# Kernel optimization log

Hardware: AMD Instinct MI355X
Metric: run time of the kernel (lower is better)

## Reference

```python
import jax, jax.numpy as jnp
import numpy as np

B, C, H, W = 4, 256, 64, 64
C8 = C // 8


def setup_inputs() -> dict:
    key = jax.random.key(0)
    k1, k2, k3, k4 = jax.random.split(key, 4)
    x = jax.random.normal(k1, (B, C, H, W), dtype=jnp.float32)
    # conv1d(ks=1, bias=False) projections -> plain [out, in] matrices
    Wq = jax.random.normal(k2, (C8, C), dtype=jnp.float32) * (1.0 / np.sqrt(C))
    Wk = jax.random.normal(k3, (C8, C), dtype=jnp.float32) * (1.0 / np.sqrt(C))
    Wv = jax.random.normal(k4, (C, C), dtype=jnp.float32) * (1.0 / np.sqrt(C))
    gamma = jnp.zeros((1,), dtype=jnp.float32)
    return {"x": x, "Wq": Wq, "Wk": Wk, "Wv": Wv, "gamma": gamma}


def reference(x, Wq, Wk, Wv, gamma):
    b, c, h, w = x.shape
    xf = x.reshape(b, c, h * w)                      # [B, C, N]
    f = jnp.einsum('oc,bcn->bon', Wq, xf)            # [B, C/8, N] query
    g = jnp.einsum('oc,bcn->bon', Wk, xf)            # [B, C/8, N] key
    hv = jnp.einsum('oc,bcn->bon', Wv, xf)           # [B, C,   N] value
    # scores[b,i,j] = sum_c f[b,c,i] * g[b,c,j]; softmax over dim=1 (i)
    scores = jnp.einsum('bci,bcj->bij', f, g)        # [B, N, N]
    beta = jax.nn.softmax(scores, axis=1)
    # o[b,c,j] = sum_i hv[b,c,i] * beta[b,i,j]
    o = jnp.einsum('bci,bij->bcj', hv, beta)         # [B, C, N]
    out = gamma[0] * o + xf
    return out.reshape(b, c, h, w)
```

## Files before the change

### kernel.cpp

```cpp
#include <hip/hip_runtime.h>

#define B_  4
#define C_  256
#define C8_ 32
#define N_  4096
#define HVS_ (N_ + 64)

#define TJ 128
#define KI 128
#define SPLITS 4

typedef __attribute__((ext_vector_type(8)))  short bf16x8;
typedef __attribute__((ext_vector_type(16))) float f32x16;

union FragAB { bf16x8 v; unsigned short u[8]; };

__device__ __forceinline__ unsigned short f2bf(float x) {
    unsigned u = __float_as_uint(x);
    unsigned r = u + 0x7FFFu + ((u >> 16) & 1u);
    return (unsigned short)(r >> 16);
}
__device__ __forceinline__ unsigned pack2bf(float a, float b) {
    return (unsigned)f2bf(a) | ((unsigned)f2bf(b) << 16);
}
__device__ __forceinline__ unsigned cvtpk(float lo, float hi) {
    unsigned r;
    asm("v_cvt_pk_bf16_f32 %0, %1, %2" : "=v"(r) : "v"(lo), "v"(hi));
    return r;
}

__global__ __launch_bounds__(256) void prep_w_kernel(
    const float* __restrict__ Wq, const float* __restrict__ Wk,
    const float* __restrict__ Wv, unsigned short* __restrict__ Wbf)
{
    int idx = (blockIdx.x * 256 + threadIdx.x) * 4;
    int row = idx >> 8;
    int col = idx & 255;
    const float* src; int r;
    if (row < 32)      { src = Wq; r = row;      }
    else if (row < 64) { src = Wk; r = row - 32; }
    else               { src = Wv; r = row - 64; }
    float4 v = *(const float4*)&src[r * 256 + col];
    uint2 o; o.x = pack2bf(v.x, v.y); o.y = pack2bf(v.z, v.w);
    *(uint2*)&Wbf[idx] = o;
}

__global__ __launch_bounds__(256) void prep_x_kernel(
    const float* __restrict__ x, unsigned short* __restrict__ xT)
{
    __shared__ unsigned short T[64][66];
    int t  = threadIdx.x;
    int b  = blockIdx.z;
    int c0 = blockIdx.y * 64;
    int n0 = blockIdx.x * 64;
    const float* xb = x + (size_t)b * C_ * N_;
    int n_l = t & 63, c_l = t >> 6;
#pragma unroll
    for (int q = 0; q < 16; ++q) {
        int c = c_l * 16 + q;
        T[n_l][c] = f2bf(xb[(size_t)(c0 + c) * N_ + n0 + n_l]);
    }
    __syncthreads();
    unsigned short* xTb = xT + (size_t)b * N_ * C_;
    int c_l2 = t & 63, nb = t >> 6;
#pragma unroll
    for (int q = 0; q < 16; ++q) {
        int n = nb * 16 + q;
        xTb[(size_t)(n0 + n) * C_ + c0 + c_l2] = T[n][c_l2];
    }
}

__global__ __launch_bounds__(256) void proj_mfma_kernel(
    const unsigned short* __restrict__ Wbf, const unsigned short* __restrict__ xT,
    unsigned short* __restrict__ fT, unsigned short* __restrict__ g,
    unsigned short* __restrict__ hv)
{
    int t = threadIdx.x, w = t >> 6, lane = t & 63;
    int half = lane >> 5, l31 = lane & 31;
    int b  = blockIdx.y;
    int n0 = blockIdx.x * 32;

    const unsigned short* xb = xT + ((size_t)b * N_ + n0 + l31) * C_;
    int nm = (w < 2) ? 3 : 2;
    int mt0 = w, mt1 = w + 4, mt2 = w + 8;

    f32x16 acc[3];
#pragma unroll
    for (int a = 0; a < 3; ++a) acc[a] = (f32x16)0.f;

#pragma unroll
    for (int ks = 0; ks < 16; ++ks) {
        int kofs = ks * 16 + half * 8;
        bf16x8 bfr = *(const bf16x8*)&xb[kofs];
        bf16x8 a0 = *(const bf16x8*)&Wbf[(size_t)(mt0 * 32 + l31) * 256 + kofs];
        acc[0] = __builtin_amdgcn_mfma_f32_32x32x16_bf16(a0, bfr, acc[0], 0, 0, 0);
        bf16x8 a1 = *(const bf16x8*)&Wbf[(size_t)(mt1 * 32 + l31) * 256 + kofs];
        acc[1] = __builtin_amdgcn_mfma_f32_32x32x16_bf16(a1, bfr, acc[1], 0, 0, 0);
        if (nm == 3) {
            bf16x8 a2 = *(const bf16x8*)&Wbf[(size_t)(mt2 * 32 + l31) * 256 + kofs];
            acc[2] = __builtin_amdgcn_mfma_f32_32x32x16_bf16(a2, bfr, acc[2], 0, 0, 0);
        }
    }

    unsigned short* fTb = fT + (size_t)b * N_ * C8_;
    unsigned short* gb  = g  + (size_t)b * C8_ * N_;
    unsigned short* hb  = hv + (size_t)b * C_  * HVS_;
#pragma unroll
    for (int im = 0; im < 3; ++im) {
        if (im >= nm) break;
        int mt = (im == 0) ? mt0 : (im == 1) ? mt1 : mt2;
        if (mt == 0) {
#pragma unroll
            for (int rp = 0; rp < 8; ++rp) {
                int r = 2 * rp;
                int R = (r & 3) + 8 * (r >> 2) + 4 * half;
                unsigned u = pack2bf(acc[0][r], acc[0][r + 1]);
                *(unsigned*)&fTb[(size_t)(n0 + l31) * C8_ + R] = u;
            }
        } else {
#pragma unroll
            for (int r = 0; r < 16; ++r) {
                int R = mt * 32 + (r & 3) + 8 * (r >> 2) + 4 * half;
                unsigned short v = f2bf(acc[im][r]);
                if (R < 64) gb[(size_t)(R - 32) * N_ + n0 + l31] = v;
                else        hb[(size_t)(R - 64) * HVS_ + n0 + l31] = v;
            }
        }
    }
}

__global__ __launch_bounds__(256, 2) void flash_kernel(
    const unsigned short* __restrict__ fT, const unsigned short* __restrict__ g,
    const unsigned short* __restrict__ hv, unsigned short* __restrict__ o_part,
    float* __restrict__ l_part)
{
    __shared__ unsigned short pT[TJ * KI];

    int t = threadIdx.x, w = t >> 6, lane = t & 63;
    int half = lane >> 5, l31 = lane & 31;

    int d  = blockIdx.x;
    int jb = (d >> 3) & 31;
    int p  = (d & 7) | (((d >> 8) & 1) << 3);
    int b  = p & 3;
    int s  = p >> 2;
    int j0 = jb * TJ;

    const unsigned short* fb = fT + (size_t)b * N_ * C8_;
    const unsigned short* gb = g  + (size_t)b * C8_ * N_;
    const unsigned short* hb = hv + (size_t)b * C_  * HVS_;

    FragAB gf[2];
#pragma unroll
    for (int ks = 0; ks < 2; ++ks)
#pragma unroll
        for (int r = 0; r < 8; ++r) {
            int ch = ks * 16 + half * 8 + r;
            gf[ks].u[r] = gb[(size_t)ch * N_ + j0 + w * 32 + l31];
        }

    f32x16 acc[8];
#pragma unroll
    for (int a = 0; a < 8; ++a) acc[a] = (f32x16)0.f;
    float lacc = 0.f;

    const int swz = (l31 & 15) << 4;
    const unsigned pbase = (unsigned)(w * 32 + l31) * (KI * 2);
    char* pTc = (char*)pT;

    const unsigned short* h0 = hb + (size_t)(w * 64 + l31) * HVS_ + half * 8;
    const unsigned short* h1 = h0 + (size_t)32 * HVS_;

    int i_begin = s * (N_ / SPLITS);

    for (int ii = 0; ii < N_ / SPLITS; ii += KI) {
        int i0 = i_begin + ii;

#pragma unroll
        for (int it = 0; it < 4; ++it) {
            const unsigned short* fr = fb + (size_t)(i0 + it * 32 + l31) * C8_ + half * 8;
            bf16x8 a0 = *(const bf16x8*)fr;
            bf16x8 a1 = *(const bf16x8*)(fr + 16);
            f32x16 sacc = (f32x16)0.f;
            sacc = __builtin_amdgcn_mfma_f32_32x32x16_bf16(a0, gf[0].v, sacc, 0, 0, 0);
            sacc = __builtin_amdgcn_mfma_f32_32x32x16_bf16(a1, gf[1].v, sacc, 0, 0, 0);
            float pv[16];
#pragma unroll
            for (int r = 0; r < 16; ++r) {
                pv[r] = __expf(sacc[r]);
                lacc += pv[r];
            }
#pragma unroll
            for (int a = 0; a < 4; ++a) {
                uint2 u;
                u.x = cvtpk(pv[4 * a + 0], pv[4 * a + 1]);
                u.y = cvtpk(pv[4 * a + 2], pv[4 * a + 3]);
                int ib = ((it * 64 + a * 16) ^ swz) + half * 8;
                *(uint2*)(pTc + pbase + ib) = u;
            }
        }
        __syncthreads();

        const unsigned short* hp0 = h0 + i0;
        const unsigned short* hp1 = h1 + i0;
#pragma unroll
        for (int ks = 0; ks < 8; ++ks) {
            bf16x8 ah0 = *(const bf16x8*)(hp0 + ks * 16);
            bf16x8 ah1 = *(const bf16x8*)(hp1 + ks * 16);
            int ib = (ks * 32 + half * 16) ^ swz;
            bf16x8 bp[4];
#pragma unroll
            for (int jt = 0; jt < 4; ++jt)
                bp[jt] = *(const bf16x8*)(pTc + (jt * 32 + l31) * (KI * 2) + ib);
#pragma unroll
            for (int jt = 0; jt < 4; ++jt) {
                acc[jt]     = __builtin_amdgcn_mfma_f32_32x32x16_bf16(ah0, bp[jt], acc[jt], 0, 0, 0);
                acc[4 + jt] = __builtin_amdgcn_mfma_f32_32x32x16_bf16(ah1, bp[jt], acc[4 + jt], 0, 0, 0);
            }
        }
        __syncthreads();
    }

    unsigned short* ob = o_part + (size_t)(b * SPLITS + s) * C_ * N_;
#pragma unroll
    for (int ct = 0; ct < 2; ++ct)
#pragma unroll
        for (int jt = 0; jt < 4; ++jt) {
            f32x16 a = acc[ct * 4 + jt];
#pragma unroll
            for (int rp = 0; rp < 8; ++rp) {
                int r = 2 * rp;
                unsigned u = cvtpk(a[r], a[r + 1]);
                int c = w * 64 + ct * 32 + (r & 3) + 8 * (r >> 2) + 4 * half;
                size_t base = (size_t)c * N_ + j0 + jt * 32 + l31;
                ob[base]      = (unsigned short)(u & 0xffffu);
                ob[base + N_] = (unsigned short)(u >> 16);
            }
        }
    float lsum = lacc + __shfl_down(lacc, 32);
    if (lane < 32)
        l_part[(size_t)(b * SPLITS + s) * N_ + j0 + w * 32 + lane] = lsum;
}

__global__ __launch_bounds__(256) void combine_kernel(
    const unsigned short* __restrict__ o_part, const float* __restrict__ l_part,
    const float* __restrict__ x, const float* __restrict__ gamma,
    float* __restrict__ out)
{
    int j = (blockIdx.x * 256 + threadIdx.x) * 4;
    int b = blockIdx.z;
    float4 l4 = {0.f, 0.f, 0.f, 0.f};
#pragma unroll
    for (int s = 0; s < SPLITS; ++s) {
        float4 lv = *(const float4*)&l_part[(size_t)(b * SPLITS + s) * N_ + j];
        l4.x += lv.x; l4.y += lv.y; l4.z += lv.z; l4.w += lv.w;
    }
    float4 inv = {1.f / l4.x, 1.f / l4.y, 1.f / l4.z, 1.f / l4.w};
    float gm = gamma[0];
#pragma unroll
    for (int cc = 0; cc < 4; ++cc) {
        int c = blockIdx.y * 4 + cc;
        float4 o = {0.f, 0.f, 0.f, 0.f};
#pragma unroll
        for (int s = 0; s < SPLITS; ++s) {
            uint2 u = *(const uint2*)&o_part[((size_t)(b * SPLITS + s) * C_ + c) * N_ + j];
            o.x += __uint_as_float(u.x << 16);
            o.y += __uint_as_float(u.x & 0xffff0000u);
            o.z += __uint_as_float(u.y << 16);
            o.w += __uint_as_float(u.y & 0xffff0000u);
        }
        size_t idx = ((size_t)b * C_ + c) * N_ + j;
        float4 xv = *(const float4*)&x[idx];
        float4 st = {gm * o.x * inv.x + xv.x, gm * o.y * inv.y + xv.y,
                     gm * o.z * inv.z + xv.z, gm * o.w * inv.w + xv.w};
        *(float4*)&out[idx] = st;
    }
}

extern "C" void kernel_launch(void* const* d_in, const int* in_sizes, int n_in,
                              void* d_out, int out_size, void* d_ws, size_t ws_size,
                              hipStream_t stream) {
    const float* x     = (const float*)d_in[0];
    const float* Wq    = (const float*)d_in[1];
    const float* Wk    = (const float*)d_in[2];
    const float* Wv    = (const float*)d_in[3];
    const float* gamma = (const float*)d_in[4];
    float* out = (float*)d_out;

    char* ws = (char*)d_ws;
    unsigned short* o_part = (unsigned short*)ws;
    float* l_part = (float*)(o_part + (size_t)SPLITS * B_ * C_ * N_);
    unsigned short* fT  = (unsigned short*)(l_part + (size_t)SPLITS * B_ * N_);
    unsigned short* g   = fT  + (size_t)B_ * C8_ * N_;
    unsigned short* hv  = g   + (size_t)B_ * C8_ * N_;
    unsigned short* Wbf = hv  + (size_t)B_ * C_  * HVS_;
    unsigned short* xT  = Wbf + (size_t)(C_ + 2 * C8_) * C_;

    prep_w_kernel<<<dim3(80), 256, 0, stream>>>(Wq, Wk, Wv, Wbf);
    prep_x_kernel<<<dim3(N_ / 64, C_ / 64, B_), 256, 0, stream>>>(x, xT);

    proj_mfma_kernel<<<dim3(N_ / 32, B_), 256, 0, stream>>>(Wbf, xT, fT, g, hv);

    flash_kernel<<<dim3(512), 256, 0, stream>>>(fT, g, hv, o_part, l_part);

    combine_kernel<<<dim3(N_ / 1024, C_ / 4, B_), 256, 0, stream>>>(o_part, l_part, x, gamma, out);
}
```

Measured before the change: 160.0 us.

## Retile flash kernel to 64-column blocks with double-buffered P and packed output

Halves the attention j-tile to 64 columns, which doubles the block count to 1024, and splits waves so that each computes half of the score tile. The P tile is double-buffered in shared memory, so each iteration needs one barrier instead of two, and value fragments are preloaded into registers before the barrier. An s_setprio hint is set around the MFMA loop. Partial outputs are stored as packed bf16 pairs of channels so the stores and the combine loads are wider. The prep and projection kernels also get vectorized transpose stores and hoisted x-fragment loads. Smaller tiles reload the value data more often and raise register pressure.

Measured after the change: 175.7 us. 1.1x slower.

```diff
diff --git a/kernel.cpp b/kernel.cpp
--- a/kernel.cpp
+++ b/kernel.cpp
@@ -6,7 +6,7 @@
 #define N_  4096
 #define HVS_ (N_ + 64)
 
-#define TJ 128
+#define TJ 64
 #define KI 128
 #define SPLITS 4
 
@@ -62,11 +62,15 @@
     }
     __syncthreads();
     unsigned short* xTb = xT + (size_t)b * N_ * C_;
-    int c_l2 = t & 63, nb = t >> 6;
-#pragma unroll
-    for (int q = 0; q < 16; ++q) {
-        int n = nb * 16 + q;
-        xTb[(size_t)(n0 + n) * C_ + c0 + c_l2] = T[n][c_l2];
+    int c4 = (t & 15) * 4;
+    int nbase = t >> 4;
+#pragma unroll
+    for (int q = 0; q < 4; ++q) {
+        int n = nbase + 16 * q;
+        uint2 u;
+        u.x = (unsigned)T[n][c4]     | ((unsigned)T[n][c4 + 1] << 16);
+        u.y = (unsigned)T[n][c4 + 2] | ((unsigned)T[n][c4 + 3] << 16);
+        *(uint2*)&xTb[(size_t)(n0 + n) * C_ + c0 + c4] = u;
     }
 }
 
@@ -84,6 +88,11 @@
     int nm = (w < 2) ? 3 : 2;
     int mt0 = w, mt1 = w + 4, mt2 = w + 8;
 
+    bf16x8 bfr[16];
+#pragma unroll
+    for (int ks = 0; ks < 16; ++ks)
+        bfr[ks] = *(const bf16x8*)&xb[ks * 16 + half * 8];
+
     f32x16 acc[3];
 #pragma unroll
     for (int a = 0; a < 3; ++a) acc[a] = (f32x16)0.f;
@@ -91,14 +100,13 @@
 #pragma unroll
     for (int ks = 0; ks < 16; ++ks) {
         int kofs = ks * 16 + half * 8;
-        bf16x8 bfr = *(const bf16x8*)&xb[kofs];
         bf16x8 a0 = *(const bf16x8*)&Wbf[(size_t)(mt0 * 32 + l31) * 256 + kofs];
-        acc[0] = __builtin_amdgcn_mfma_f32_32x32x16_bf16(a0, bfr, acc[0], 0, 0, 0);
+        acc[0] = __builtin_amdgcn_mfma_f32_32x32x16_bf16(a0, bfr[ks], acc[0], 0, 0, 0);
         bf16x8 a1 = *(const bf16x8*)&Wbf[(size_t)(mt1 * 32 + l31) * 256 + kofs];
-        acc[1] = __builtin_amdgcn_mfma_f32_32x32x16_bf16(a1, bfr, acc[1], 0, 0, 0);
+        acc[1] = __builtin_amdgcn_mfma_f32_32x32x16_bf16(a1, bfr[ks], acc[1], 0, 0, 0);
         if (nm == 3) {
             bf16x8 a2 = *(const bf16x8*)&Wbf[(size_t)(mt2 * 32 + l31) * 256 + kofs];
-            acc[2] = __builtin_amdgcn_mfma_f32_32x32x16_bf16(a2, bfr, acc[2], 0, 0, 0);
+            acc[2] = __builtin_amdgcn_mfma_f32_32x32x16_bf16(a2, bfr[ks], acc[2], 0, 0, 0);
         }
     }
 
@@ -131,17 +139,19 @@
 
 __global__ __launch_bounds__(256, 2) void flash_kernel(
     const unsigned short* __restrict__ fT, const unsigned short* __restrict__ g,
-    const unsigned short* __restrict__ hv, unsigned short* __restrict__ o_part,
+    const unsigned short* __restrict__ hv, unsigned* __restrict__ o_part,
     float* __restrict__ l_part)
 {
-    __shared__ unsigned short pT[TJ * KI];
+    __shared__ unsigned short pT[2][TJ * KI];
 
     int t = threadIdx.x, w = t >> 6, lane = t & 63;
     int half = lane >> 5, l31 = lane & 31;
+    int wj = w & 1;
+    int wi = w >> 1;
 
     int d  = blockIdx.x;
-    int jb = (d >> 3) & 31;
-    int p  = (d & 7) | (((d >> 8) & 1) << 3);
+    int jb = (d >> 3) & 63;
+    int p  = (d & 7) | (((d >> 9) & 1) << 3);
     int b  = p & 3;
     int s  = p >> 2;
     int j0 = jb * TJ;
@@ -156,29 +166,41 @@
 #pragma unroll
         for (int r = 0; r < 8; ++r) {
             int ch = ks * 16 + half * 8 + r;
-            gf[ks].u[r] = gb[(size_t)ch * N_ + j0 + w * 32 + l31];
-        }
-
-    f32x16 acc[8];
-#pragma unroll
-    for (int a = 0; a < 8; ++a) acc[a] = (f32x16)0.f;
+            gf[ks].u[r] = gb[(size_t)ch * N_ + j0 + wj * 32 + l31];
+        }
+
+    f32x16 acc[4];
+#pragma unroll
+    for (int a = 0; a < 4; ++a) acc[a] = (f32x16)0.f;
     float lacc = 0.f;
 
     const int swz = (l31 & 15) << 4;
-    const unsigned pbase = (unsigned)(w * 32 + l31) * (KI * 2);
-    char* pTc = (char*)pT;
+    const unsigned pbaseA = (unsigned)(wj * 32 + l31) * (KI * 2);
+    const int colbase0 = wi * 128;
 
     const unsigned short* h0 = hb + (size_t)(w * 64 + l31) * HVS_ + half * 8;
     const unsigned short* h1 = h0 + (size_t)32 * HVS_;
 
     int i_begin = s * (N_ / SPLITS);
 
-    for (int ii = 0; ii < N_ / SPLITS; ii += KI) {
-        int i0 = i_begin + ii;
-
-#pragma unroll
-        for (int it = 0; it < 4; ++it) {
-            const unsigned short* fr = fb + (size_t)(i0 + it * 32 + l31) * C8_ + half * 8;
+    for (int kit = 0; kit < (N_ / SPLITS) / KI; ++kit) {
+        int i0 = i_begin + kit * KI;
+
+        const unsigned short* hp0 = h0 + i0;
+        const unsigned short* hp1 = h1 + i0;
+        bf16x8 hv0[8], hv1[8];
+#pragma unroll
+        for (int ks = 0; ks < 8; ++ks) {
+            hv0[ks] = *(const bf16x8*)(hp0 + ks * 16);
+            hv1[ks] = *(const bf16x8*)(hp1 + ks * 16);
+        }
+
+        char* pTc = (char*)pT[kit & 1];
+
+#pragma unroll
+        for (int it = 0; it < 2; ++it) {
+            const unsigned short* fr =
+                fb + (size_t)(i0 + wi * 64 + it * 32 + l31) * C8_ + half * 8;
             bf16x8 a0 = *(const bf16x8*)fr;
             bf16x8 a1 = *(const bf16x8*)(fr + 16);
             f32x16 sacc = (f32x16)0.f;
@@ -186,64 +208,66 @@
             sacc = __builtin_amdgcn_mfma_f32_32x32x16_bf16(a1, gf[1].v, sacc, 0, 0, 0);
             float pv[16];
 #pragma unroll
-            for (int r = 0; r < 16; ++r) {
-                pv[r] = __expf(sacc[r]);
-                lacc += pv[r];
-            }
+            for (int r = 0; r < 16; ++r) pv[r] = __expf(sacc[r]);
+            float s0 = (pv[0]  + pv[1])  + (pv[2]  + pv[3]);
+            float s1 = (pv[4]  + pv[5])  + (pv[6]  + pv[7]);
+            float s2 = (pv[8]  + pv[9])  + (pv[10] + pv[11]);
+            float s3 = (pv[12] + pv[13]) + (pv[14] + pv[15]);
+            lacc += (s0 + s1) + (s2 + s3);
 #pragma unroll
             for (int a = 0; a < 4; ++a) {
                 uint2 u;
                 u.x = cvtpk(pv[4 * a + 0], pv[4 * a + 1]);
                 u.y = cvtpk(pv[4 * a + 2], pv[4 * a + 3]);
-                int ib = ((it * 64 + a * 16) ^ swz) + half * 8;
-                *(uint2*)(pTc + pbase + ib) = u;
+                int ib = ((colbase0 + it * 64 + a * 16) ^ swz) + half * 8;
+                *(uint2*)(pTc + pbaseA + ib) = u;
             }
         }
-        __syncthreads();
-
-        const unsigned short* hp0 = h0 + i0;
-        const unsigned short* hp1 = h1 + i0;
+
+        asm volatile("s_waitcnt lgkmcnt(0)" ::: "memory");
+        __builtin_amdgcn_s_barrier();
+        asm volatile("" ::: "memory");
+
+        __builtin_amdgcn_s_setprio(1);
 #pragma unroll
         for (int ks = 0; ks < 8; ++ks) {
-            bf16x8 ah0 = *(const bf16x8*)(hp0 + ks * 16);
-            bf16x8 ah1 = *(const bf16x8*)(hp1 + ks * 16);
             int ib = (ks * 32 + half * 16) ^ swz;
-            bf16x8 bp[4];
-#pragma unroll
-            for (int jt = 0; jt < 4; ++jt)
-                bp[jt] = *(const bf16x8*)(pTc + (jt * 32 + l31) * (KI * 2) + ib);
-#pragma unroll
-            for (int jt = 0; jt < 4; ++jt) {
-                acc[jt]     = __builtin_amdgcn_mfma_f32_32x32x16_bf16(ah0, bp[jt], acc[jt], 0, 0, 0);
-                acc[4 + jt] = __builtin_amdgcn_mfma_f32_32x32x16_bf16(ah1, bp[jt], acc[4 + jt], 0, 0, 0);
-            }
-        }
-        __syncthreads();
-    }
-
-    unsigned short* ob = o_part + (size_t)(b * SPLITS + s) * C_ * N_;
+            bf16x8 bp0 = *(const bf16x8*)(pTc + (size_t)l31 * (KI * 2) + ib);
+            bf16x8 bp1 = *(const bf16x8*)(pTc + (size_t)(32 + l31) * (KI * 2) + ib);
+            acc[0] = __builtin_amdgcn_mfma_f32_32x32x16_bf16(hv0[ks], bp0, acc[0], 0, 0, 0);
+            acc[1] = __builtin_amdgcn_mfma_f32_32x32x16_bf16(hv0[ks], bp1, acc[1], 0, 0, 0);
+            acc[2] = __builtin_amdgcn_mfma_f32_32x32x16_bf16(hv1[ks], bp0, acc[2], 0, 0, 0);
+            acc[3] = __builtin_amdgcn_mfma_f32_32x32x16_bf16(hv1[ks], bp1, acc[3], 0, 0, 0);
+        }
+        __builtin_amdgcn_s_setprio(0);
+    }
+
+    float lsum = lacc + __shfl_down(lacc, 32);
+    __syncthreads();
+    float* lred = (float*)pT;
+    if (lane < 32) lred[wi * 64 + wj * 32 + lane] = lsum;
+    __syncthreads();
+    if (t < 64)
+        l_part[(size_t)(b * SPLITS + s) * N_ + j0 + t] = lred[t] + lred[64 + t];
+
+    unsigned* ob = o_part + (size_t)(b * SPLITS + s) * (C_ / 2) * N_;
 #pragma unroll
     for (int ct = 0; ct < 2; ++ct)
 #pragma unroll
-        for (int jt = 0; jt < 4; ++jt) {
-            f32x16 a = acc[ct * 4 + jt];
+        for (int jt = 0; jt < 2; ++jt) {
+            f32x16 a = acc[ct * 2 + jt];
 #pragma unroll
             for (int rp = 0; rp < 8; ++rp) {
                 int r = 2 * rp;
                 unsigned u = cvtpk(a[r], a[r + 1]);
                 int c = w * 64 + ct * 32 + (r & 3) + 8 * (r >> 2) + 4 * half;
-                size_t base = (size_t)c * N_ + j0 + jt * 32 + l31;
-                ob[base]      = (unsigned short)(u & 0xffffu);
-                ob[base + N_] = (unsigned short)(u >> 16);
+                ob[(size_t)(c >> 1) * N_ + j0 + jt * 32 + l31] = u;
             }
         }
-    float lsum = lacc + __shfl_down(lacc, 32);
-    if (lane < 32)
-        l_part[(size_t)(b * SPLITS + s) * N_ + j0 + w * 32 + lane] = lsum;
 }
 
 __global__ __launch_bounds__(256) void combine_kernel(
-    const unsigned short* __restrict__ o_part, const float* __restrict__ l_part,
+    const unsigned* __restrict__ o_part, const float* __restrict__ l_part,
     const float* __restrict__ x, const float* __restrict__ gamma,
     float* __restrict__ out)
 {
@@ -258,22 +282,26 @@
     float4 inv = {1.f / l4.x, 1.f / l4.y, 1.f / l4.z, 1.f / l4.w};
     float gm = gamma[0];
 #pragma unroll
-    for (int cc = 0; cc < 4; ++cc) {
-        int c = blockIdx.y * 4 + cc;
-        float4 o = {0.f, 0.f, 0.f, 0.f};
+    for (int cc = 0; cc < 2; ++cc) {
+        int c2 = blockIdx.y * 2 + cc;
+        float4 olo = {0.f, 0.f, 0.f, 0.f}, ohi = {0.f, 0.f, 0.f, 0.f};
 #pragma unroll
         for (int s = 0; s < SPLITS; ++s) {
-            uint2 u = *(const uint2*)&o_part[((size_t)(b * SPLITS + s) * C_ + c) * N_ + j];
-            o.x += __uint_as_float(u.x << 16);
-            o.y += __uint_as_float(u.x & 0xffff0000u);
-            o.z += __uint_as_float(u.y << 16);
-            o.w += __uint_as_float(u.y & 0xffff0000u);
-        }
-        size_t idx = ((size_t)b * C_ + c) * N_ + j;
-        float4 xv = *(const float4*)&x[idx];
-        float4 st = {gm * o.x * inv.x + xv.x, gm * o.y * inv.y + xv.y,
-                     gm * o.z * inv.z + xv.z, gm * o.w * inv.w + xv.w};
-        *(float4*)&out[idx] = st;
+            uint4 u = *(const uint4*)&o_part[((size_t)(b * SPLITS + s) * (C_ / 2) + c2) * N_ + j];
+            olo.x += __uint_as_float(u.x << 16); ohi.x += __uint_as_float(u.x & 0xffff0000u);
+            olo.y += __uint_as_float(u.y << 16); ohi.y += __uint_as_float(u.y & 0xffff0000u);
+            olo.z += __uint_as_float(u.z << 16); ohi.z += __uint_as_float(u.z & 0xffff0000u);
+            olo.w += __uint_as_float(u.w << 16); ohi.w += __uint_as_float(u.w & 0xffff0000u);
+        }
+        size_t i0 = ((size_t)b * C_ + 2 * c2) * N_ + j;
+        float4 x0 = *(const float4*)&x[i0];
+        float4 x1 = *(const float4*)&x[i0 + N_];
+        float4 r0 = {gm * olo.x * inv.x + x0.x, gm * olo.y * inv.y + x0.y,
+                     gm * olo.z * inv.z + x0.z, gm * olo.w * inv.w + x0.w};
+        float4 r1 = {gm * ohi.x * inv.x + x1.x, gm * ohi.y * inv.y + x1.y,
+                     gm * ohi.z * inv.z + x1.z, gm * ohi.w * inv.w + x1.w};
+        *(float4*)&out[i0] = r0;
+        *(float4*)&out[i0 + N_] = r1;
     }
 }
 
@@ -288,8 +316,8 @@
     float* out = (float*)d_out;
 
     char* ws = (char*)d_ws;
-    unsigned short* o_part = (unsigned short*)ws;
-    float* l_part = (float*)(o_part + (size_t)SPLITS * B_ * C_ * N_);
+    unsigned* o_part = (unsigned*)ws;
+    float* l_part = (float*)(o_part + (size_t)SPLITS * B_ * (C_ / 2) * N_);
     unsigned short* fT  = (unsigned short*)(l_part + (size_t)SPLITS * B_ * N_);
     unsigned short* g   = fT  + (size_t)B_ * C8_ * N_;
     unsigned short* hv  = g   + (size_t)B_ * C8_ * N_;
@@ -301,7 +329,7 @@
 
     proj_mfma_kernel<<<dim3(N_ / 32, B_), 256, 0, stream>>>(Wbf, xT, fT, g, hv);
 
-    flash_kernel<<<dim3(512), 256, 0, stream>>>(fT, g, hv, o_part, l_part);
+    flash_kernel<<<dim3((N_ / TJ) * B_ * SPLITS), 256, 0, stream>>>(fT, g, hv, o_part, l_part);
 
     combine_kernel<<<dim3(N_ / 1024, C_ / 4, B_), 256, 0, stream>>>(o_part, l_part, x, gamma, out);
 }
```
